# Kernel optimization log

Hardware: AMD Instinct MI355X
Metric: run time of the kernel (lower is better)

## Reference

```python
import jax, jax.numpy as jnp
import numpy as np

N_NODES = 50000
NEG_SLOPE = 0.2


def gat_layer(x, src, dst, edge_attr, W, a_src, a_dst, We, a_edge, b, n):
    """PyG GATConv (heads=1, concat=True, add_self_loops=True, fill_value='mean')."""
    h = x @ W                                   # [N, C] shared lin for src/dst
    alpha_s = h @ a_src                          # [N]
    alpha_d = h @ a_dst                          # [N]
    # self loops; self-loop edge_attr = mean of incoming edge_attr per node
    deg = jax.ops.segment_sum(jnp.ones_like(dst, dtype=edge_attr.dtype), dst, num_segments=n)
    ea_mean = jax.ops.segment_sum(edge_attr, dst, num_segments=n) / jnp.maximum(deg, 1.0)[:, None]
    loop = jnp.arange(n, dtype=src.dtype)
    s = jnp.concatenate([src, loop])             # [E+N]
    d = jnp.concatenate([dst, loop])
    ea = jnp.concatenate([edge_attr, ea_mean], axis=0)
    alpha_e = (ea @ We) @ a_edge                 # [E+N]
    alpha = jax.nn.leaky_relu(alpha_s[s] + alpha_d[d] + alpha_e, NEG_SLOPE)
    # segment softmax over destination neighborhoods (self-loops guarantee non-empty)
    amax = jax.ops.segment_max(alpha, d, num_segments=n)
    ealpha = jnp.exp(alpha - amax[d])
    denom = jax.ops.segment_sum(ealpha, d, num_segments=n)
    coef = ealpha / denom[d]                     # [E+N]
    out = jax.ops.segment_sum(h[s] * coef[:, None], d, num_segments=n)
    return out + b


def setup_inputs() -> dict:
    key = jax.random.key(0)
    ks = jax.random.split(key, 16)
    N, E, F_in, H, C, ED = N_NODES, 800000, 256, 128, 128, 60
    inp = {
        "x": jax.random.normal(ks[0], (N, F_in), jnp.float32),
        "edge_index": jax.random.randint(ks[1], (2, E), 0, N, jnp.int32),
        "edge_features": jax.random.normal(ks[2], (E, ED), jnp.float32),
        "batch_size": 16,
    }
    def glorot(k, shape):
        fan = shape[0] + (shape[1] if len(shape) > 1 else 1)
        return jax.random.normal(k, shape, jnp.float32) * np.sqrt(2.0 / fan)
    # layer 1
    inp["W1"] = glorot(ks[3], (F_in, H))
    inp["a_src1"] = glorot(ks[4], (H,))
    inp["a_dst1"] = glorot(ks[5], (H,))
    inp["We1"] = glorot(ks[6], (ED, H))
    inp["a_edge1"] = glorot(ks[7], (H,))
    inp["b1"] = jnp.zeros((H,), jnp.float32)
    # layer 2
    inp["W2"] = glorot(ks[8], (H, C))
    inp["a_src2"] = glorot(ks[9], (C,))
    inp["a_dst2"] = glorot(ks[10], (C,))
    inp["We2"] = glorot(ks[11], (ED, C))
    inp["a_edge2"] = glorot(ks[12], (C,))
    inp["b2"] = jnp.zeros((C,), jnp.float32)
    return inp


def reference(x, edge_index, edge_features, batch_size,
              W1, a_src1, a_dst1, We1, a_edge1, b1,
              W2, a_src2, a_dst2, We2, a_edge2, b2):
    n = x.shape[0]
    src, dst = edge_index[0], edge_index[1]
    h = gat_layer(x, src, dst, edge_features, W1, a_src1, a_dst1, We1, a_edge1, b1, n)
    h = jax.nn.relu(h)
    z = gat_layer(h, src, dst, edge_features, W2, a_src2, a_dst2, We2, a_edge2, b2, n)
    # decode: gather-dot over labeled edge pairs
    res = jnp.sum(z[src] * z[dst], axis=-1)      # [E]
    half = res.shape[0] // 2
    res_half = res[:half] + res[half:]
    return res_half.reshape((batch_size, -1))
```

## Files before the change

### kernel.cpp

```cpp
#include <hip/hip_runtime.h>
#include <hip/hip_bf16.h>

typedef __attribute__((ext_vector_type(8))) short short8;
typedef __attribute__((ext_vector_type(4))) float floatx4;

__device__ __forceinline__ float lrelu(float a){ return a > 0.f ? a : 0.2f * a; }
__device__ __forceinline__ float bflo(unsigned u){ return __uint_as_float(u << 16); }
__device__ __forceinline__ float bfhi(unsigned u){ return __uint_as_float(u & 0xffff0000u); }
__device__ __forceinline__ unsigned short f2bf(float f){
  __hip_bfloat16 h = __float2bfloat16(f);
  return *reinterpret_cast<unsigned short*>(&h);
}
__device__ __forceinline__ float dot4(float4 a, float4 b){
  return a.x*b.x + a.y*b.y + a.z*b.z + a.w*b.w;
}

__global__ __launch_bounds__(256) void k_prep(const int* __restrict__ src, const int* __restrict__ dst,
                       int* __restrict__ degi, int* __restrict__ sdeg,
                       int* __restrict__ eslot, int* __restrict__ sslot, int E, int CB,
                       const float* __restrict__ We1, const float* __restrict__ ae1,
                       const float* __restrict__ We2, const float* __restrict__ ae2,
                       float* __restrict__ we1, float* __restrict__ we2,
                       const float* __restrict__ W1, unsigned short* __restrict__ W1t,
                       const float* __restrict__ W2, unsigned short* __restrict__ W2t) {
  int t = threadIdx.x;
  if (blockIdx.x < (unsigned)CB) {
    int e = blockIdx.x * 256 + t;
    if (e < E) {
      eslot[e] = atomicAdd(degi + dst[e], 1);
      sslot[e] = atomicAdd(sdeg + src[e], 1);
    }
    return;
  }
  int b = blockIdx.x - CB;
  if (b == 0) {
    if (t >= 64) return;
    float s1 = 0.f, s2 = 0.f;
    if (t < 60) {
      const float4* r1 = reinterpret_cast<const float4*>(We1 + t * 128);
      const float4* r2 = reinterpret_cast<const float4*>(We2 + t * 128);
      const float4* a1 = reinterpret_cast<const float4*>(ae1);
      const float4* a2 = reinterpret_cast<const float4*>(ae2);
      for (int i = 0; i < 32; ++i) {
        float4 x1 = r1[i], y1 = a1[i];
        float4 x2 = r2[i], y2 = a2[i];
        s1 += x1.x*y1.x + x1.y*y1.y + x1.z*y1.z + x1.w*y1.w;
        s2 += x2.x*y2.x + x2.y*y2.y + x2.z*y2.z + x2.w*y2.w;
      }
    }
    we1[t] = s1; we2[t] = s2;
  } else if (b <= 128) {
    int idx = (b - 1) * 256 + t;
    int k = idx >> 7, n = idx & 127;
    W1t[(size_t)n * 256 + k] = f2bf(W1[idx]);
  } else {
    int idx = (b - 129) * 256 + t;
    int k = idx >> 7, n = idx & 127;
    W2t[(size_t)n * 128 + k] = f2bf(W2[idx]);
  }
}

__device__ __forceinline__ void scan_body(const int* __restrict__ degi, int* __restrict__ rowptr,
                                          int N, int E) {
  __shared__ int wsums[16];
  int t = threadIdx.x;
  int wave = t >> 6, lane = t & 63;
  const int CH = 52;
  int lo = t * CH;
  int v[52];
  int s = 0;
  #pragma unroll
  for (int i = 0; i < 13; ++i) {
    int base_i = lo + 4 * i;
    if (base_i + 4 <= N) {
      int4 q = *reinterpret_cast<const int4*>(degi + base_i);
      v[4*i+0] = q.x; v[4*i+1] = q.y; v[4*i+2] = q.z; v[4*i+3] = q.w;
      s += q.x + q.y + q.z + q.w;
    } else {
      #pragma unroll
      for (int j = 0; j < 4; ++j) {
        int idx = base_i + j;
        int x = (idx < N) ? degi[idx] : 0;
        v[4*i+j] = x; s += x;
      }
    }
  }
  int inc = s;
  #pragma unroll
  for (int off = 1; off < 64; off <<= 1) {
    int u = __shfl_up(inc, off);
    if (lane >= off) inc += u;
  }
  if (lane == 63) wsums[wave] = inc;
  __syncthreads();
  if (wave == 0) {
    int ws = (lane < 16) ? wsums[lane] : 0;
    #pragma unroll
    for (int off = 1; off < 16; off <<= 1) {
      int u = __shfl_up(ws, off);
      if (lane >= off) ws += u;
    }
    if (lane < 16) wsums[lane] = ws;
  }
  __syncthreads();
  int base = inc - s + (wave ? wsums[wave - 1] : 0);
  #pragma unroll
  for (int i = 0; i < 13; ++i) {
    int base_i = lo + 4 * i;
    if (base_i + 4 <= N) {
      int4 o;
      o.x = base; base += v[4*i+0];
      o.y = base; base += v[4*i+1];
      o.z = base; base += v[4*i+2];
      o.w = base; base += v[4*i+3];
      *reinterpret_cast<int4*>(rowptr + base_i) = o;
    } else {
      #pragma unroll
      for (int j = 0; j < 4; ++j) {
        int idx = base_i + j;
        if (idx < N) { rowptr[idx] = base; base += v[4*i+j]; }
      }
    }
  }
  if (t == 0) rowptr[N] = E;
}

__global__ __launch_bounds__(1024) void k_scanedot(const int* __restrict__ degi, int* __restrict__ rowptr,
                       const int* __restrict__ sdeg, int* __restrict__ srowptr,
                       int N, int E,
                       const float* __restrict__ ef,
                       const float* __restrict__ we1, const float* __restrict__ we2,
                       float2* __restrict__ edgeD, int EDOTB) {
  if (blockIdx.x == 0) { scan_body(degi, rowptr, N, E); return; }
  if (blockIdx.x == 1) { scan_body(sdeg, srowptr, N, E); return; }
  int t = threadIdx.x;
  int sub = t & 3;
  int qw = (int)(blockIdx.x - 2) * 256 + (t >> 2);
  const float4* w1v = reinterpret_cast<const float4*>(we1);
  const float4* w2v = reinterpret_cast<const float4*>(we2);
  float4 wa0 = w1v[sub],     wb0 = w2v[sub];
  float4 wa1 = w1v[sub + 4], wb1 = w2v[sub + 4];
  float4 wa2 = w1v[sub + 8], wb2 = w2v[sub + 8];
  bool has3 = sub < 3;
  float4 wa3 = make_float4(0.f,0.f,0.f,0.f), wb3 = wa3;
  if (has3) { wa3 = w1v[sub + 12]; wb3 = w2v[sub + 12]; }
  const float4* efq = reinterpret_cast<const float4*>(ef);
  int stride = EDOTB * 256;
  for (int e = qw; e < E; e += stride) {
    size_t b = (size_t)e * 15;
    float4 f0 = efq[b + sub];
    float4 f1 = efq[b + sub + 4];
    float4 f2 = efq[b + sub + 8];
    float4 f3 = make_float4(0.f,0.f,0.f,0.f);
    if (has3) f3 = efq[b + sub + 12];
    float d1 = dot4(f0, wa0) + dot4(f1, wa1) + dot4(f2, wa2) + dot4(f3, wa3);
    float d2 = dot4(f0, wb0) + dot4(f1, wb1) + dot4(f2, wb2) + dot4(f3, wb3);
    d1 += __shfl_xor(d1, 1); d1 += __shfl_xor(d1, 2);
    d2 += __shfl_xor(d2, 1); d2 += __shfl_xor(d2, 2);
    if (sub == 0) edgeD[e] = make_float2(d1, d2);
  }
}

template <int K, bool AFP32>
__device__ __forceinline__ void gemm_body(int wid, int lane,
    const void* __restrict__ Av, const unsigned short* __restrict__ Bt,
    unsigned short* __restrict__ C,
    const float* __restrict__ a_src, const float* __restrict__ a_dst,
    float* __restrict__ alps, float* __restrict__ alpd, int M) {
  int mt = wid;
  if (mt * 16 >= M) return;
  int r = lane & 15, quad = lane >> 4;
  int m = mt * 16 + r;
  floatx4 acc[8] = {};
  for (int k0 = 0; k0 < K; k0 += 32) {
    int kk = k0 + quad * 8;
    short8 a;
    if (AFP32) {
      const float4* ap = reinterpret_cast<const float4*>((const float*)Av + (size_t)m * K + kk);
      float4 lo = ap[0], hi = ap[1];
      union { short8 v; unsigned short u[8]; } pa;
      pa.u[0]=f2bf(lo.x); pa.u[1]=f2bf(lo.y); pa.u[2]=f2bf(lo.z); pa.u[3]=f2bf(lo.w);
      pa.u[4]=f2bf(hi.x); pa.u[5]=f2bf(hi.y); pa.u[6]=f2bf(hi.z); pa.u[7]=f2bf(hi.w);
      a = pa.v;
    } else {
      a = *reinterpret_cast<const short8*>((const unsigned short*)Av + (size_t)m * K + kk);
    }
    #pragma unroll
    for (int t = 0; t < 8; ++t) {
      short8 b = *reinterpret_cast<const short8*>(Bt + (size_t)(t*16 + r) * K + kk);
      acc[t] = __builtin_amdgcn_mfma_f32_16x16x32_bf16(a, b, acc[t], 0, 0, 0);
    }
  }
  float asv[8], adv[8];
  #pragma unroll
  for (int t = 0; t < 8; ++t) {
    int col = t * 16 + r;
    asv[t] = a_src[col]; adv[t] = a_dst[col];
  }
  #pragma unroll
  for (int rr = 0; rr < 4; ++rr) {
    float ps = 0.f, pd = 0.f;
    #pragma unroll
    for (int t = 0; t < 8; ++t) { ps += acc[t][rr] * asv[t]; pd += acc[t][rr] * adv[t]; }
    #pragma unroll
    for (int mo = 1; mo <= 8; mo <<= 1) { ps += __shfl_xor(ps, mo); pd += __shfl_xor(pd, mo); }
    if (r == 0) {
      int row = mt * 16 + quad * 4 + rr;
      alps[row] = ps;
      alpd[row] = pd;
    }
  }
  #pragma unroll
  for (int t = 0; t < 8; ++t) {
    int col = t * 16 + r;
    #pragma unroll
    for (int rr = 0; rr < 4; ++rr) {
      int row = mt * 16 + quad * 4 + rr;
      C[(size_t)row * 128 + col] = f2bf(acc[t][rr]);
    }
  }
}

template <int K, bool AFP32>
__global__ __launch_bounds__(256) void k_gemm(const void* __restrict__ Av, const unsigned short* __restrict__ Bt,
                                              unsigned short* __restrict__ C,
                                              const float* __restrict__ a_src, const float* __restrict__ a_dst,
                                              float* __restrict__ alps, float* __restrict__ alpd, int M) {
  int wid = (blockIdx.x * 256 + threadIdx.x) >> 6;
  int lane = threadIdx.x & 63;
  gemm_body<K, AFP32>(wid, lane, Av, Bt, C, a_src, a_dst, alps, alpd, M);
}

__global__ __launch_bounds__(256) void k_scatgemm(
                       const int* __restrict__ src, const int* __restrict__ dst,
                       const int* __restrict__ eslot, const int* __restrict__ rowptr,
                       const int* __restrict__ sslot, const int* __restrict__ srowptr,
                       const float2* __restrict__ edgeD, float4* __restrict__ csr,
                       uint2* __restrict__ sedge,
                       int E, int half, int GB,
                       const float* __restrict__ x, const unsigned short* __restrict__ W1t,
                       unsigned short* __restrict__ hA,
                       const float* __restrict__ a_src, const float* __restrict__ a_dst,
                       float* __restrict__ alps, float* __restrict__ alpd, int N) {
  int t = threadIdx.x;
  if (blockIdx.x < (unsigned)GB) {
    int wid = (blockIdx.x * 256 + t) >> 6;
    int lane = t & 63;
    gemm_body<256, true>(wid, lane, x, W1t, hA, a_src, a_dst, alps, alpd, N);
    return;
  }
  int e = (blockIdx.x - GB) * 256 + t;
  if (e >= E) return;
  int s = src[e], d = dst[e];
  float2 dd = edgeD[e];
  int slot = rowptr[d] + eslot[e];
  float4 v;
  v.x = __int_as_float(s); v.y = dd.x; v.z = dd.y; v.w = 0.f;
  csr[slot] = v;
  int ss = srowptr[s] + sslot[e];
  int outidx = (e < half) ? e : e - half;
  uint2 rec;
  rec.x = (unsigned)s | ((unsigned)d << 16);
  rec.y = (unsigned)outidx;
  sedge[ss] = rec;
}

__global__ __launch_bounds__(256) void k_agg(const int* __restrict__ rowptr, const float4* __restrict__ csr,
                      const float* __restrict__ as_, const float* __restrict__ ad_,
                      const unsigned short* __restrict__ h, const float* __restrict__ bias,
                      unsigned short* __restrict__ out, int N, int use2, int do_relu) {
  int i = (blockIdx.x * blockDim.x + threadIdx.x) >> 6;
  int lane = threadIdx.x & 63;
  if (i >= N) return;
  int st = lane >> 4;
  int q  = lane & 15;
  int start = rowptr[i], end = rowptr[i + 1];
  int cnt = end - start;
  float adi = ad_[i], asi = as_[i];
  float m = -3.0e38f, s = 0.f, esum = 0.f;
  float acc[8] = {};
  int idx = start + st;
  float4 cur, nx1, nx2;
  float as_c = 0.f, as_1 = 0.f;
  uint4 hv_c, hv_1;
  if (idx < end) cur = csr[idx];
  if (idx + 4 < end) nx1 = csr[idx + 4];
  if (idx + 8 < end) nx2 = csr[idx + 8];
  if (idx < end) {
    int sv = __float_as_int(cur.x);
    as_c = as_[sv];
    hv_c = *reinterpret_cast<const uint4*>(h + (size_t)sv * 128 + q * 8);
  }
  if (idx + 4 < end) {
    int sv = __float_as_int(nx1.x);
    as_1 = as_[sv];
    hv_1 = *reinterpret_cast<const uint4*>(h + (size_t)sv * 128 + q * 8);
  }
  for (; idx < end; idx += 4) {
    float4 n3;
    if (idx + 12 < end) n3 = csr[idx + 12];
    float as_2 = 0.f; uint4 hv_2;
    if (idx + 8 < end) {
      int sv = __float_as_int(nx2.x);
      as_2 = as_[sv];
      hv_2 = *reinterpret_cast<const uint4*>(h + (size_t)sv * 128 + q * 8);
    }
    float e = use2 ? cur.z : cur.y;
    float a = lrelu(as_c + adi + e);
    esum += e;
    if (a > m + 8.f) {
      float rr = __expf(m - a);
      s *= rr;
      #pragma unroll
      for (int j = 0; j < 8; ++j) acc[j] *= rr;
      m = a;
    }
    float w = __expf(a - m);
    s += w;
    acc[0] += w * bflo(hv_c.x); acc[1] += w * bfhi(hv_c.x);
    acc[2] += w * bflo(hv_c.y); acc[3] += w * bfhi(hv_c.y);
    acc[4] += w * bflo(hv_c.z); acc[5] += w * bfhi(hv_c.z);
    acc[6] += w * bflo(hv_c.w); acc[7] += w * bfhi(hv_c.w);
    cur = nx1; nx1 = nx2; nx2 = n3;
    as_c = as_1; hv_c = hv_1;
    as_1 = as_2; hv_1 = hv_2;
  }
  #pragma unroll
  for (int off = 16; off <= 32; off <<= 1) {
    float m_o = __shfl_xor(m, off);
    float s_o = __shfl_xor(s, off);
    float e_o = __shfl_xor(esum, off);
    float ao[8];
    #pragma unroll
    for (int j = 0; j < 8; ++j) ao[j] = __shfl_xor(acc[j], off);
    float Mn = fmaxf(m, m_o);
    float f  = __expf(m - Mn), fo = __expf(m_o - Mn);
    s = s * f + s_o * fo;
    #pragma unroll
    for (int j = 0; j < 8; ++j) acc[j] = acc[j] * f + ao[j] * fo;
    esum += e_o;
    m = Mn;
  }
  float a_self = lrelu(asi + adi + esum / fmaxf((float)cnt, 1.f));
  float M2 = fmaxf(m, a_self);
  float g = __expf(m - M2);
  float w_self = __expf(a_self - M2);
  s = s * g + w_self;
  uint4 hs = *reinterpret_cast<const uint4*>(h + (size_t)i * 128 + q * 8);
  float hsf[8] = { bflo(hs.x), bfhi(hs.x), bflo(hs.y), bfhi(hs.y),
                   bflo(hs.z), bfhi(hs.z), bflo(hs.w), bfhi(hs.w) };
  #pragma unroll
  for (int j = 0; j < 8; ++j) acc[j] = acc[j] * g + w_self * hsf[j];
  float inv = 1.0f / s;
  float4 bv0 = *reinterpret_cast<const float4*>(bias + q * 8);
  float4 bv1 = *reinterpret_cast<const float4*>(bias + q * 8 + 4);
  float o[8];
  o[0] = acc[0]*inv + bv0.x; o[1] = acc[1]*inv + bv0.y;
  o[2] = acc[2]*inv + bv0.z; o[3] = acc[3]*inv + bv0.w;
  o[4] = acc[4]*inv + bv1.x; o[5] = acc[5]*inv + bv1.y;
  o[6] = acc[6]*inv + bv1.z; o[7] = acc[7]*inv + bv1.w;
  if (do_relu) {
    #pragma unroll
    for (int j = 0; j < 8; ++j) o[j] = fmaxf(o[j], 0.f);
  }
  if (st == 0) {
    uint4 ov;
    ov.x = (unsigned)f2bf(o[0]) | ((unsigned)f2bf(o[1]) << 16);
    ov.y = (unsigned)f2bf(o[2]) | ((unsigned)f2bf(o[3]) << 16);
    ov.z = (unsigned)f2bf(o[4]) | ((unsigned)f2bf(o[5]) << 16);
    ov.w = (unsigned)f2bf(o[6]) | ((unsigned)f2bf(o[7]) << 16);
    *reinterpret_cast<uint4*>(out + (size_t)i * 128 + q * 8) = ov;
  }
}

__global__ __launch_bounds__(256) void k_decode_sorted(const uint2* __restrict__ sedge,
                         const unsigned short* __restrict__ z, float* __restrict__ out, int E) {
  int j = (blockIdx.x * 256 + threadIdx.x) >> 3;
  if (j >= E) return;
  int q = threadIdx.x & 7;
  uint2 rec = sedge[j];
  int s = rec.x & 0xffff;
  int d = rec.x >> 16;
  const uint4* za = reinterpret_cast<const uint4*>(z + (size_t)s * 128 + q * 16);
  const uint4* zb = reinterpret_cast<const uint4*>(z + (size_t)d * 128 + q * 16);
  uint4 a0 = za[0], a1 = za[1];
  uint4 b0 = zb[0], b1 = zb[1];
  float p = bflo(a0.x)*bflo(b0.x) + bfhi(a0.x)*bfhi(b0.x)
          + bflo(a0.y)*bflo(b0.y) + bfhi(a0.y)*bfhi(b0.y)
          + bflo(a0.z)*bflo(b0.z) + bfhi(a0.z)*bfhi(b0.z)
          + bflo(a0.w)*bflo(b0.w) + bfhi(a0.w)*bfhi(b0.w)
          + bflo(a1.x)*bflo(b1.x) + bfhi(a1.x)*bfhi(b1.x)
          + bflo(a1.y)*bflo(b1.y) + bfhi(a1.y)*bfhi(b1.y)
          + bflo(a1.z)*bflo(b1.z) + bfhi(a1.z)*bfhi(b1.z)
          + bflo(a1.w)*bflo(b1.w) + bfhi(a1.w)*bfhi(b1.w);
  p += __shfl_xor(p, 1);
  p += __shfl_xor(p, 2);
  p += __shfl_xor(p, 4);
  if (q == 0) atomicAdd(out + rec.y, p);
}

extern "C" void kernel_launch(void* const* d_in, const int* in_sizes, int n_in,
                              void* d_out, int out_size, void* d_ws, size_t ws_size,
                              hipStream_t stream) {
  const int H = 128;
  const int N = in_sizes[0] / 256;
  const int E = in_sizes[1] / 2;
  const int half = E / 2;

  const float* x   = (const float*)d_in[0];
  const int* eidx  = (const int*)d_in[1];
  const float* ef  = (const float*)d_in[2];
  const float* W1  = (const float*)d_in[4];
  const float* as1 = (const float*)d_in[5];
  const float* ad1 = (const float*)d_in[6];
  const float* We1 = (const float*)d_in[7];
  const float* ae1 = (const float*)d_in[8];
  const float* b1  = (const float*)d_in[9];
  const float* W2  = (const float*)d_in[10];
  const float* as2 = (const float*)d_in[11];
  const float* ad2 = (const float*)d_in[12];
  const float* We2 = (const float*)d_in[13];
  const float* ae2 = (const float*)d_in[14];
  const float* b2  = (const float*)d_in[15];

  const int* src = eidx;
  const int* dst = eidx + E;

  size_t off = 0;
  auto alloc = [&](size_t bytes) -> void* {
    void* p = (char*)d_ws + off;
    off += (bytes + 255) & ~(size_t)255;
    return p;
  };
  float*  we1    = (float*)alloc(64 * 4);
  float*  we2    = (float*)alloc(64 * 4);
  int*    degs   = (int*)alloc((size_t)N * 4 * 2);
  int*    degi   = degs;
  int*    sdeg   = degs + N;
  float*  alps   = (float*)alloc((size_t)N * 4);
  float*  alpd   = (float*)alloc((size_t)N * 4);
  int*    eslot  = (int*)alloc((size_t)E * 4);
  int*    sslot  = (int*)alloc((size_t)E * 4);
  int*    rowptr = (int*)alloc((size_t)(N + 1) * 4);
  int*    srowptr= (int*)alloc((size_t)(N + 1) * 4);
  float2* edgeD  = (float2*)alloc((size_t)E * 8);
  float4* csr    = (float4*)alloc((size_t)E * 16);
  uint2*  sedge  = (uint2*)alloc((size_t)E * 8);
  unsigned short* W1t = (unsigned short*)alloc((size_t)128 * 256 * 2);
  unsigned short* W2t = (unsigned short*)alloc((size_t)128 * 128 * 2);
  unsigned short* hA  = (unsigned short*)alloc((size_t)N * H * 2);
  unsigned short* hB  = (unsigned short*)alloc((size_t)N * H * 2);

  hipMemsetAsync(degs, 0, (size_t)N * 8, stream);
  hipMemsetAsync(d_out, 0, (size_t)out_size, stream);

  int CB = (E + 255) / 256;
  k_prep<<<CB + 193, 256, 0, stream>>>(src, dst, degi, sdeg, eslot, sslot, E, CB,
                                       We1, ae1, We2, ae2, we1, we2, W1, W1t, W2, W2t);

  int EDOTB = 782;
  k_scanedot<<<2 + EDOTB, 1024, 0, stream>>>(degi, rowptr, sdeg, srowptr, N, E,
                                             ef, we1, we2, edgeD, EDOTB);

  int gwaves = (N + 15) / 16;
  int GB = (gwaves + 3) / 4;
  int SB = (E + 255) / 256;
  k_scatgemm<<<GB + SB, 256, 0, stream>>>(src, dst, eslot, rowptr, sslot, srowptr,
                                          edgeD, csr, sedge, E, half, GB,
                                          x, W1t, hA, as1, ad1, alps, alpd, N);
  k_agg<<<(N + 3) / 4, 256, 0, stream>>>(rowptr, csr, alps, alpd, hA, b1, hB, N, 0, 1);
  k_gemm<128, false><<<GB, 256, 0, stream>>>(hB, W2t, hA, as2, ad2, alps, alpd, N);
  k_agg<<<(N + 3) / 4, 256, 0, stream>>>(rowptr, csr, alps, alpd, hA, b2, hB, N, 1, 0);
  int DB = (E * 8 + 255) / 256;
  k_decode_sorted<<<DB, 256, 0, stream>>>(sedge, hB, (float*)d_out, E);
}
```

Measured before the change: 605.4 us.

## Decode edges through destination CSR instead of a separate source-sorted edge list

Removes the second (source-keyed) counting sort: no src-degree atomics, no second scan and no sedge scatter. The output index is packed into the unused w field of the existing dst-CSR record. The decode becomes one wavefront per destination node. It loads z[i] once and walks the CSR neighbours with prefetching, reducing each dot product over 16 lanes. The cost is per-edge atomics onto the output in neighbour order and load imbalance across nodes with different degrees.

```diff
diff --git a/kernel.cpp b/kernel.cpp
--- a/kernel.cpp
+++ b/kernel.cpp
@@ -15,9 +15,8 @@
   return a.x*b.x + a.y*b.y + a.z*b.z + a.w*b.w;
 }
 
-__global__ __launch_bounds__(256) void k_prep(const int* __restrict__ src, const int* __restrict__ dst,
-                       int* __restrict__ degi, int* __restrict__ sdeg,
-                       int* __restrict__ eslot, int* __restrict__ sslot, int E, int CB,
+__global__ __launch_bounds__(256) void k_prep(const int* __restrict__ dst, int* __restrict__ degi,
+                       int* __restrict__ eslot, int E, int CB,
                        const float* __restrict__ We1, const float* __restrict__ ae1,
                        const float* __restrict__ We2, const float* __restrict__ ae2,
                        float* __restrict__ we1, float* __restrict__ we2,
@@ -26,10 +25,7 @@
   int t = threadIdx.x;
   if (blockIdx.x < (unsigned)CB) {
     int e = blockIdx.x * 256 + t;
-    if (e < E) {
-      eslot[e] = atomicAdd(degi + dst[e], 1);
-      sslot[e] = atomicAdd(sdeg + src[e], 1);
-    }
+    if (e < E) eslot[e] = atomicAdd(degi + dst[e], 1);
     return;
   }
   int b = blockIdx.x - CB;
@@ -126,16 +122,14 @@
 }
 
 __global__ __launch_bounds__(1024) void k_scanedot(const int* __restrict__ degi, int* __restrict__ rowptr,
-                       const int* __restrict__ sdeg, int* __restrict__ srowptr,
                        int N, int E,
                        const float* __restrict__ ef,
                        const float* __restrict__ we1, const float* __restrict__ we2,
                        float2* __restrict__ edgeD, int EDOTB) {
   if (blockIdx.x == 0) { scan_body(degi, rowptr, N, E); return; }
-  if (blockIdx.x == 1) { scan_body(sdeg, srowptr, N, E); return; }
   int t = threadIdx.x;
   int sub = t & 3;
-  int qw = (int)(blockIdx.x - 2) * 256 + (t >> 2);
+  int qw = (int)(blockIdx.x - 1) * 256 + (t >> 2);
   const float4* w1v = reinterpret_cast<const float4*>(we1);
   const float4* w2v = reinterpret_cast<const float4*>(we2);
   float4 wa0 = w1v[sub],     wb0 = w2v[sub];
@@ -234,9 +228,7 @@
 __global__ __launch_bounds__(256) void k_scatgemm(
                        const int* __restrict__ src, const int* __restrict__ dst,
                        const int* __restrict__ eslot, const int* __restrict__ rowptr,
-                       const int* __restrict__ sslot, const int* __restrict__ srowptr,
                        const float2* __restrict__ edgeD, float4* __restrict__ csr,
-                       uint2* __restrict__ sedge,
                        int E, int half, int GB,
                        const float* __restrict__ x, const unsigned short* __restrict__ W1t,
                        unsigned short* __restrict__ hA,
@@ -251,18 +243,13 @@
   }
   int e = (blockIdx.x - GB) * 256 + t;
   if (e >= E) return;
-  int s = src[e], d = dst[e];
+  int d = dst[e];
   float2 dd = edgeD[e];
   int slot = rowptr[d] + eslot[e];
+  int outidx = (e < half) ? e : e - half;
   float4 v;
-  v.x = __int_as_float(s); v.y = dd.x; v.z = dd.y; v.w = 0.f;
+  v.x = __int_as_float(src[e]); v.y = dd.x; v.z = dd.y; v.w = __int_as_float(outidx);
   csr[slot] = v;
-  int ss = srowptr[s] + sslot[e];
-  int outidx = (e < half) ? e : e - half;
-  uint2 rec;
-  rec.x = (unsigned)s | ((unsigned)d << 16);
-  rec.y = (unsigned)outidx;
-  sedge[ss] = rec;
 }
 
 __global__ __launch_bounds__(256) void k_agg(const int* __restrict__ rowptr, const float4* __restrict__ csr,
@@ -373,30 +360,53 @@
   }
 }
 
-__global__ __launch_bounds__(256) void k_decode_sorted(const uint2* __restrict__ sedge,
-                         const unsigned short* __restrict__ z, float* __restrict__ out, int E) {
-  int j = (blockIdx.x * 256 + threadIdx.x) >> 3;
-  if (j >= E) return;
-  int q = threadIdx.x & 7;
-  uint2 rec = sedge[j];
-  int s = rec.x & 0xffff;
-  int d = rec.x >> 16;
-  const uint4* za = reinterpret_cast<const uint4*>(z + (size_t)s * 128 + q * 16);
-  const uint4* zb = reinterpret_cast<const uint4*>(z + (size_t)d * 128 + q * 16);
-  uint4 a0 = za[0], a1 = za[1];
-  uint4 b0 = zb[0], b1 = zb[1];
-  float p = bflo(a0.x)*bflo(b0.x) + bfhi(a0.x)*bfhi(b0.x)
-          + bflo(a0.y)*bflo(b0.y) + bfhi(a0.y)*bfhi(b0.y)
-          + bflo(a0.z)*bflo(b0.z) + bfhi(a0.z)*bfhi(b0.z)
-          + bflo(a0.w)*bflo(b0.w) + bfhi(a0.w)*bfhi(b0.w)
-          + bflo(a1.x)*bflo(b1.x) + bfhi(a1.x)*bfhi(b1.x)
-          + bflo(a1.y)*bflo(b1.y) + bfhi(a1.y)*bfhi(b1.y)
-          + bflo(a1.z)*bflo(b1.z) + bfhi(a1.z)*bfhi(b1.z)
-          + bflo(a1.w)*bflo(b1.w) + bfhi(a1.w)*bfhi(b1.w);
-  p += __shfl_xor(p, 1);
-  p += __shfl_xor(p, 2);
-  p += __shfl_xor(p, 4);
-  if (q == 0) atomicAdd(out + rec.y, p);
+__global__ __launch_bounds__(256) void k_decode_csr(const int* __restrict__ rowptr,
+                         const float4* __restrict__ csr,
+                         const unsigned short* __restrict__ z,
+                         float* __restrict__ out, int N) {
+  int i = (blockIdx.x * blockDim.x + threadIdx.x) >> 6;
+  int lane = threadIdx.x & 63;
+  if (i >= N) return;
+  int st = lane >> 4;
+  int q  = lane & 15;
+  int start = rowptr[i], end = rowptr[i + 1];
+  uint4 zi = *reinterpret_cast<const uint4*>(z + (size_t)i * 128 + q * 8);
+  float zf[8] = { bflo(zi.x), bfhi(zi.x), bflo(zi.y), bfhi(zi.y),
+                  bflo(zi.z), bfhi(zi.z), bflo(zi.w), bfhi(zi.w) };
+  int idx = start + st;
+  float4 cur, nx1, nx2;
+  uint4 zv_c, zv_1;
+  if (idx < end) cur = csr[idx];
+  if (idx + 4 < end) nx1 = csr[idx + 4];
+  if (idx + 8 < end) nx2 = csr[idx + 8];
+  if (idx < end) {
+    int sv = __float_as_int(cur.x);
+    zv_c = *reinterpret_cast<const uint4*>(z + (size_t)sv * 128 + q * 8);
+  }
+  if (idx + 4 < end) {
+    int sv = __float_as_int(nx1.x);
+    zv_1 = *reinterpret_cast<const uint4*>(z + (size_t)sv * 128 + q * 8);
+  }
+  for (; idx < end; idx += 4) {
+    float4 n3;
+    if (idx + 12 < end) n3 = csr[idx + 12];
+    uint4 zv_2;
+    if (idx + 8 < end) {
+      int sv = __float_as_int(nx2.x);
+      zv_2 = *reinterpret_cast<const uint4*>(z + (size_t)sv * 128 + q * 8);
+    }
+    float p = zf[0]*bflo(zv_c.x) + zf[1]*bfhi(zv_c.x)
+            + zf[2]*bflo(zv_c.y) + zf[3]*bfhi(zv_c.y)
+            + zf[4]*bflo(zv_c.z) + zf[5]*bfhi(zv_c.z)
+            + zf[6]*bflo(zv_c.w) + zf[7]*bfhi(zv_c.w);
+    p += __shfl_xor(p, 1);
+    p += __shfl_xor(p, 2);
+    p += __shfl_xor(p, 4);
+    p += __shfl_xor(p, 8);
+    if (q == 0) atomicAdd(out + __float_as_int(cur.w), p);
+    cur = nx1; nx1 = nx2; nx2 = n3;
+    zv_c = zv_1; zv_1 = zv_2;
+  }
 }
 
 extern "C" void kernel_launch(void* const* d_in, const int* in_sizes, int n_in,
@@ -434,43 +444,35 @@
   };
   float*  we1    = (float*)alloc(64 * 4);
   float*  we2    = (float*)alloc(64 * 4);
-  int*    degs   = (int*)alloc((size_t)N * 4 * 2);
-  int*    degi   = degs;
-  int*    sdeg   = degs + N;
+  int*    degi   = (int*)alloc((size_t)N * 4);
   float*  alps   = (float*)alloc((size_t)N * 4);
   float*  alpd   = (float*)alloc((size_t)N * 4);
   int*    eslot  = (int*)alloc((size_t)E * 4);
-  int*    sslot  = (int*)alloc((size_t)E * 4);
   int*    rowptr = (int*)alloc((size_t)(N + 1) * 4);
-  int*    srowptr= (int*)alloc((size_t)(N + 1) * 4);
   float2* edgeD  = (float2*)alloc((size_t)E * 8);
   float4* csr    = (float4*)alloc((size_t)E * 16);
-  uint2*  sedge  = (uint2*)alloc((size_t)E * 8);
   unsigned short* W1t = (unsigned short*)alloc((size_t)128 * 256 * 2);
   unsigned short* W2t = (unsigned short*)alloc((size_t)128 * 128 * 2);
   unsigned short* hA  = (unsigned short*)alloc((size_t)N * H * 2);
   unsigned short* hB  = (unsigned short*)alloc((size_t)N * H * 2);
 
-  hipMemsetAsync(degs, 0, (size_t)N * 8, stream);
+  hipMemsetAsync(degi, 0, (size_t)N * 4, stream);
   hipMemsetAsync(d_out, 0, (size_t)out_size, stream);
 
   int CB = (E + 255) / 256;
-  k_prep<<<CB + 193, 256, 0, stream>>>(src, dst, degi, sdeg, eslot, sslot, E, CB,
+  k_prep<<<CB + 193, 256, 0, stream>>>(dst, degi, eslot, E, CB,
                                        We1, ae1, We2, ae2, we1, we2, W1, W1t, W2, W2t);
 
   int EDOTB = 782;
-  k_scanedot<<<2 + EDOTB, 1024, 0, stream>>>(degi, rowptr, sdeg, srowptr, N, E,
-                                             ef, we1, we2, edgeD, EDOTB);
+  k_scanedot<<<1 + EDOTB, 1024, 0, stream>>>(degi, rowptr, N, E, ef, we1, we2, edgeD, EDOTB);
 
   int gwaves = (N + 15) / 16;
   int GB = (gwaves + 3) / 4;
   int SB = (E + 255) / 256;
-  k_scatgemm<<<GB + SB, 256, 0, stream>>>(src, dst, eslot, rowptr, sslot, srowptr,
-                                          edgeD, csr, sedge, E, half, GB,
+  k_scatgemm<<<GB + SB, 256, 0, stream>>>(src, dst, eslot, rowptr, edgeD, csr, E, half, GB,
                                           x, W1t, hA, as1, ad1, alps, alpd, N);
   k_agg<<<(N + 3) / 4, 256, 0, stream>>>(rowptr, csr, alps, alpd, hA, b1, hB, N, 0, 1);
   k_gemm<128, false><<<GB, 256, 0, stream>>>(hB, W2t, hA, as2, ad2, alps, alpd, N);
   k_agg<<<(N + 3) / 4, 256, 0, stream>>>(rowptr, csr, alps, alpd, hA, b2, hB, N, 1, 0);
-  int DB = (E * 8 + 255) / 256;
-  k_decode_sorted<<<DB, 256, 0, stream>>>(sedge, hB, (float*)d_out, E);
-}
+  k_decode_csr<<<(N + 3) / 4, 256, 0, stream>>>(rowptr, csr, hB, (float*)d_out, N);
+}
```

After: 563.2 us. 7.0% less time.
